# Kernel tuning notes

Hardware: AMD Instinct MI355X
Metric: run time of the kernel (lower is better)

## Reference

```python
import jax, jax.numpy as jnp
import numpy as np

B, L, D, H, DFF, C = 16, 1024, 256, 4, 2048, 3
NS, NC = 4, 4
DH = D // H


def _ln(x, g, b):
    m = x.mean(-1, keepdims=True)
    v = ((x - m) ** 2).mean(-1, keepdims=True)
    return (x - m) / jnp.sqrt(v + 1e-5) * g + b


def setup_inputs() -> dict:
    key = jax.random.key(0)
    ks = jax.random.split(key, 24)
    n = lambda k, s: jax.random.normal(k, s, jnp.float32) * 0.02
    return {
        'shape_idxs': jax.random.randint(ks[0], (B, L), 0, NS, jnp.int32),
        'color_idxs': jax.random.randint(ks[1], (B, L), 0, NC, jnp.int32),
        'shape_emb': n(ks[2], (NS, D)),
        'color_emb': n(ks[3], (NC, D)),
        'Wq': n(ks[4], (D, D)), 'bq': jnp.zeros((D,)),
        'Wk': n(ks[5], (D, D)), 'bk': jnp.zeros((D,)),
        'Wv': n(ks[6], (D, D)), 'bv': jnp.zeros((D,)),
        'Wo': n(ks[7], (D, D)), 'bo': jnp.zeros((D,)),
        'g1': jnp.ones((D,)), 'be1': jnp.zeros((D,)),
        'W1': n(ks[8], (D, DFF)), 'bf1': jnp.zeros((DFF,)),
        'W2': n(ks[9], (DFF, D)), 'bf2': jnp.zeros((D,)),
        'g2': jnp.ones((D,)), 'be2': jnp.zeros((D,)),
        'Wl': n(ks[10], (D, C)), 'bl': jnp.zeros((C,)),
        'Wp1': n(ks[11], (D, D)), 'bp1': jnp.zeros((D,)),
        'Wp2': n(ks[12], (D, 1)), 'bp2': jnp.zeros((1,)),
        'wc': n(ks[13], (1, 1)), 'bc': jnp.zeros((1,)),
    }


def reference(shape_idxs, color_idxs, shape_emb, color_emb, Wq, bq, Wk, bk, Wv, bv,
              Wo, bo, g1, be1, W1, bf1, W2, bf2, g2, be2, Wl, bl,
              Wp1, bp1, Wp2, bp2, wc, bc):
    # embed (dropout is identity in eval)
    x = shape_emb[shape_idxs] + color_emb[color_idxs]  # [B,L,D]
    # post-norm transformer encoder layer (PyTorch default)
    heads = lambda t: t.reshape(B, L, H, DH)
    q, k, v = heads(x @ Wq + bq), heads(x @ Wk + bk), heads(x @ Wv + bv)
    scores = jnp.einsum('blhd,bmhd->bhlm', q, k) / jnp.sqrt(jnp.float32(DH))
    attn = jax.nn.softmax(scores, axis=-1)
    ctx = jnp.einsum('bhlm,bmhd->blhd', attn, v).reshape(B, L, D)
    y = _ln(x + ctx @ Wo + bo, g1, be1)
    ff = jax.nn.relu(y @ W1 + bf1) @ W2 + bf2
    y = _ln(y + ff, g2, be2)  # trans_out [B,L,D]
    # latent logits / KL(prior || probs) with batchmean reduction
    logits = y @ Wl + bl
    logp = jax.nn.log_softmax(logits, axis=-1)
    prior = 1.0 / C
    kl_loss = jnp.sum(prior * (jnp.log(jnp.float32(prior)) - logp)) / B
    # data-dependent boundary segmentation (argmax of probs == argmax of logits)
    boundaries = (jnp.argmax(logits, axis=-1) == 0)
    boundaries = boundaries.at[:, 0].set(True)
    closed = boundaries & (jnp.arange(L) > 0)  # closure at l>0 ends segment at l
    seg_id = jnp.cumsum(closed.astype(jnp.int32), axis=1) - closed  # exclusive cumsum
    gid = (jnp.arange(B)[:, None] * L + seg_id).reshape(-1)  # global segment ids
    sums = jax.ops.segment_sum(y.reshape(B * L, D), gid, num_segments=B * L)
    counts = jax.ops.segment_sum(jnp.ones((B * L,), jnp.float32), gid, num_segments=B * L)
    means = sums / jnp.maximum(counts, 1.0)[:, None]  # per-segment mean [B*L,D]
    # predicate net + composition, mean over valid segments
    preds = jax.nn.sigmoid(jax.nn.relu(means @ Wp1 + bp1) @ Wp2 + bp2)  # [B*L,1]
    comp = (preds * wc[0, 0] + bc[0]).reshape(B, L)
    valid = (counts > 0).reshape(B, L).astype(jnp.float32)
    mean_comp = jnp.sum(comp * valid, axis=1) / jnp.sum(valid, axis=1)
    final_scores = jax.nn.sigmoid(mean_comp)
    return final_scores, kl_loss
```

## Files before the change

### kernel.cpp

```cpp
#include <hip/hip_runtime.h>


typedef unsigned short u16;
typedef u16    u16x4  __attribute__((ext_vector_type(4)));
typedef u16    u16x8  __attribute__((ext_vector_type(8)));
typedef __bf16 bf16x8 __attribute__((ext_vector_type(8)));
typedef float  f32x4  __attribute__((ext_vector_type(4)));

__device__ __forceinline__ float bf2f(u16 u) {
    union { unsigned int i; float f; } v; v.i = ((unsigned int)u) << 16; return v.f;
}
__device__ __forceinline__ u16 f2bf(float f) {
    union { float f; unsigned int i; } v; v.f = f;
    unsigned int r = (v.i + 0x7FFFu + ((v.i >> 16) & 1u)) >> 16;
    return (u16)r;
}
__device__ __forceinline__ u16 f2bf_fast(float f) {
    union { __bf16 h; u16 u; } v; v.h = (__bf16)f; return v.u;
}
__device__ __forceinline__ void gll16(const u16* g, u16* l) {
    __builtin_amdgcn_global_load_lds((__attribute__((address_space(1))) void*)(u16*)g,
                                     (__attribute__((address_space(3))) void*)l, 16, 0, 0);
}
__device__ __forceinline__ int get_mode(const int* __restrict__ detp) {
    int s = 0;
#pragma unroll 8
    for (int i = 0; i < 64; ++i) s += detp[i];
    return s > 16;
}

__global__ __launch_bounds__(256) void k_detect(const u16* __restrict__ w1raw,
                                                int* __restrict__ detp) {
    int i = blockIdx.x * 256 + threadIdx.x;
    int bad = 0;
    for (int k = i; k < 65536; k += 64 * 256) {
        unsigned v = w1raw[k] & 0x7FFFu;
        if (v >= 0x7F80u) bad++;
    }
    for (int off = 32; off >= 1; off >>= 1) bad += __shfl_xor(bad, off);
    __shared__ int bs[4];
    if ((threadIdx.x & 63) == 0) bs[threadIdx.x >> 6] = bad;
    __syncthreads();
    if (threadIdx.x == 0) detp[blockIdx.x] = bs[0] + bs[1] + bs[2] + bs[3];
}
__global__ void k_sentinel_f32(float* __restrict__ out, int code) {
    int t = threadIdx.x;
    if (t < 17) out[t] = (float)code;
}

struct PrepTab {
    const void* src[7];
    u16*        dst[7];
    int         K[7], N[7];
    float       scale[7];
    int         tstart[8];
    const void* isrc[17];
    unsigned    idstoff[17];
    int         in[17];
    float       iscale[17];
    u16*        ing;
};
__global__ __launch_bounds__(256) void k_prep(PrepTab tt, const int* __restrict__ detp) {
    int m = get_mode(detp);
    int bx = blockIdx.x;
    if (bx >= tt.tstart[7]) {
        int t = bx - tt.tstart[7];
        int n = tt.in[t];
        float sc = tt.iscale[t];
        u16* dst = tt.ing + tt.idstoff[t];
        for (int i = threadIdx.x; i < n; i += 256) {
            float v = m ? ((const float*)tt.isrc[t])[i] : bf2f(((const u16*)tt.isrc[t])[i]);
            dst[i] = f2bf(v * sc);
        }
        return;
    }
    __shared__ u16 tile[32][33];
    int wgt = 0;
#pragma unroll
    for (int i = 1; i < 7; ++i) if (bx >= tt.tstart[i]) wgt = i;
    int local = bx - tt.tstart[wgt];
    int K = tt.K[wgt], N = tt.N[wgt];
    float sc = tt.scale[wgt];
    int ntx = N >> 5;
    int txt = local % ntx, tyt = local / ntx;
    const void* W = tt.src[wgt];
    u16* Wt = tt.dst[wgt];
    int tx = threadIdx.x & 31, ty = threadIdx.x >> 5;
    int n = txt * 32 + tx;
    for (int i = ty; i < 32; i += 8) {
        size_t idx = (size_t)(tyt * 32 + i) * N + n;
        float v = m ? ((const float*)W)[idx] : bf2f(((const u16*)W)[idx]);
        tile[i][tx] = f2bf(v * sc);
    }
    __syncthreads();
    int k2 = tyt * 32 + tx;
    for (int i = ty; i < 32; i += 8) {
        int n2 = txt * 32 + i;
        Wt[(size_t)n2 * K + k2] = tile[tx][i];
    }
}

__global__ __launch_bounds__(256) void k_embed(const int* __restrict__ si,
                                               const int* __restrict__ ci,
                                               const void* __restrict__ se,
                                               const void* __restrict__ ce,
                                               u16* __restrict__ X,
                                               const int* __restrict__ detp) {
    int m = get_mode(detp);
    int t = blockIdx.x * 256 + threadIdx.x;
    int row = t >> 5, seg = (t & 31) * 8;
    int s = si[row], c = ci[row];
    u16x8 o;
    if (m) {
        const float* sp = (const float*)se + s * 256 + seg;
        const float* cp = (const float*)ce + c * 256 + seg;
#pragma unroll
        for (int e = 0; e < 8; ++e) o[e] = f2bf(sp[e] + cp[e]);
    } else {
        u16x8 a = *(const u16x8*)((const u16*)se + s * 256 + seg);
        u16x8 b = *(const u16x8*)((const u16*)ce + c * 256 + seg);
#pragma unroll
        for (int e = 0; e < 8; ++e) o[e] = f2bf(bf2f(a[e]) + bf2f(b[e]));
    }
    *(u16x8*)&X[(size_t)row * 256 + seg] = o;
}

__global__ __launch_bounds__(256) void k_gemm_bt(const u16* __restrict__ A,
                                                 const u16* __restrict__ Bt,
                                                 const u16* __restrict__ bias,
                                                 u16* __restrict__ C,
                                                 int N, int K, int relu, int gx) {
    __shared__ u16 As[128][32];
    __shared__ u16 Bs[128][32];
    const int tid = threadIdx.x;
    const int xcd = blockIdx.x & 7, j = blockIdx.x >> 3;
    const int m0 = (xcd * 16 + j / gx) * 128, n0 = (j % gx) * 128;
    const int lane = tid & 63, wid = tid >> 6;
    const int wm = (wid & 1) * 64, wn = (wid >> 1) * 64;
    const int m16 = lane & 15, quad = lane >> 4;
    f32x4 acc[4][4] = {};
    const int arow = tid >> 2;
    const int ac8  = (tid & 3) * 8;
    const u16* Ap0 = A  + (size_t)(m0 + arow) * K + ac8;
    const u16* Ap1 = A  + (size_t)(m0 + 64 + arow) * K + ac8;
    const u16* Bp0 = Bt + (size_t)(n0 + arow) * K + ac8;
    const u16* Bp1 = Bt + (size_t)(n0 + 64 + arow) * K + ac8;
    u16* lA0 = &As[arow][ac8];
    u16* lA1 = &As[64 + arow][ac8];
    u16* lB0 = &Bs[arow][ac8];
    u16* lB1 = &Bs[64 + arow][ac8];

    for (int k0 = 0; k0 < K; k0 += 32) {
        __syncthreads();
        gll16(Ap0 + k0, lA0);
        gll16(Ap1 + k0, lA1);
        gll16(Bp0 + k0, lB0);
        gll16(Bp1 + k0, lB1);
        __syncthreads();
        bf16x8 af[4], bfv[4];
#pragma unroll
        for (int i = 0; i < 4; ++i)
            af[i] = *(const bf16x8*)&As[wm + i * 16 + m16][quad * 8];
#pragma unroll
        for (int j2 = 0; j2 < 4; ++j2)
            bfv[j2] = *(const bf16x8*)&Bs[wn + j2 * 16 + m16][quad * 8];
#pragma unroll
        for (int i = 0; i < 4; ++i)
#pragma unroll
            for (int j2 = 0; j2 < 4; ++j2)
                acc[i][j2] = __builtin_amdgcn_mfma_f32_16x16x32_bf16(
                    af[i], bfv[j2], acc[i][j2], 0, 0, 0);
    }

#pragma unroll
    for (int i = 0; i < 4; ++i) {
        int row = m0 + wm + i * 16 + quad * 4;
#pragma unroll
        for (int j2 = 0; j2 < 4; ++j2) {
            int col = n0 + wn + j2 * 16 + m16;
            float bv = bf2f(bias[col]);
#pragma unroll
            for (int r = 0; r < 4; ++r) {
                float v = acc[i][j2][r] + bv;
                if (relu) v = fmaxf(v, 0.f);
                C[(size_t)(row + r) * N + col] = f2bf_fast(v);
            }
        }
    }
}

__global__ __launch_bounds__(256) void k_gemm64(const u16* __restrict__ A,
                                                const u16* __restrict__ Bt,
                                                const u16* __restrict__ bias,
                                                u16* __restrict__ C,
                                                int N, int K, int relu,
                                                int gx, int mtpx,
                                                u16* __restrict__ vt) {
    __shared__ u16 As0[64][32], As1[64][32];
    __shared__ u16 Bs0[128][32], Bs1[128][32];
    const int tid = threadIdx.x;
    const int xcd = blockIdx.x & 7, j = blockIdx.x >> 3;
    const int m0 = (xcd * mtpx + j / gx) * 64, n0 = (j % gx) * 128;
    const int vmode = (vt != nullptr) && (n0 >= 512);
    const int lane = tid & 63, wid = tid >> 6;
    const int wm = (wid & 1) * 32, wn = (wid >> 1) * 64;
    const int m16 = lane & 15, quad = lane >> 4;
    f32x4 acc[2][4] = {};
    const int arow = tid >> 2;
    const int ac8  = (tid & 3) * 8;
    const u16* Ap  = A  + (size_t)(m0 + arow) * K + ac8;
    const u16* Bp0 = Bt + (size_t)(n0 + arow) * K + ac8;
    const u16* Bp1 = Bt + (size_t)(n0 + 64 + arow) * K + ac8;
    u16* lA0  = &As0[arow][ac8];
    u16* lA1  = &As1[arow][ac8];
    u16* lB00 = &Bs0[arow][ac8];
    u16* lB01 = &Bs0[64 + arow][ac8];
    u16* lB10 = &Bs1[arow][ac8];
    u16* lB11 = &Bs1[64 + arow][ac8];

    for (int k0 = 0; k0 < K; k0 += 64) {
        __syncthreads();
        gll16(Ap + k0,        lA0);
        gll16(Ap + k0 + 32,   lA1);
        gll16(Bp0 + k0,       lB00);
        gll16(Bp0 + k0 + 32,  lB10);
        gll16(Bp1 + k0,       lB01);
        gll16(Bp1 + k0 + 32,  lB11);
        __syncthreads();
#pragma unroll
        for (int ks = 0; ks < 2; ++ks) {
            bf16x8 af[2], bfv[4];
#pragma unroll
            for (int i = 0; i < 2; ++i)
                af[i] = ks == 0 ? *(const bf16x8*)&As0[wm + i * 16 + m16][quad * 8]
                                : *(const bf16x8*)&As1[wm + i * 16 + m16][quad * 8];
#pragma unroll
            for (int j2 = 0; j2 < 4; ++j2)
                bfv[j2] = ks == 0 ? *(const bf16x8*)&Bs0[wn + j2 * 16 + m16][quad * 8]
                                  : *(const bf16x8*)&Bs1[wn + j2 * 16 + m16][quad * 8];
#pragma unroll
            for (int i = 0; i < 2; ++i)
#pragma unroll
                for (int j2 = 0; j2 < 4; ++j2)
                    acc[i][j2] = __builtin_amdgcn_mfma_f32_16x16x32_bf16(
                        af[i], bfv[j2], acc[i][j2], 0, 0, 0);
        }
    }

#pragma unroll
    for (int i = 0; i < 2; ++i) {
        int row = m0 + wm + i * 16 + quad * 4;
#pragma unroll
        for (int j2 = 0; j2 < 4; ++j2) {
            int col = n0 + wn + j2 * 16 + m16;
            float bv = bf2f(bias[col]);
            if (vmode) {
                int ch = col - 512;
                u16x4 o;
#pragma unroll
                for (int r = 0; r < 4; ++r) o[r] = f2bf_fast(acc[i][j2][r] + bv);
                size_t vb = ((size_t)((row >> 10) * 4 + (ch >> 6)) * 64 + (ch & 63)) * 1024
                          + (row & 1023);
                *(u16x4*)&vt[vb] = o;
            } else {
#pragma unroll
                for (int r = 0; r < 4; ++r) {
                    float v = acc[i][j2][r] + bv;
                    if (relu) v = fmaxf(v, 0.f);
                    C[(size_t)(row + r) * N + col] = f2bf_fast(v);
                }
            }
        }
    }
}

__global__ __launch_bounds__(256) void k_gemm64n(const u16* __restrict__ A,
                                                 const u16* __restrict__ Bt,
                                                 const u16* __restrict__ bias,
                                                 u16* __restrict__ C,
                                                 int N, int K, int relu,
                                                 int gnx, int mtpx,
                                                 const float* __restrict__ gate) {
    __shared__ u16 As0[64][32], As1[64][32];
    __shared__ u16 Bs0[64][32], Bs1[64][32];
    const int tid = threadIdx.x;
    const int xcd = blockIdx.x & 7, j = blockIdx.x >> 3;
    const int m0 = (xcd * mtpx + j / gnx) * 64, n0 = (j % gnx) * 64;
    if (gate && gate[m0] == 0.f) return;
    const int lane = tid & 63, w = tid >> 6;
    const int m16 = lane & 15, quad = lane >> 4;
    f32x4 acc[4] = {};
    const int arow = tid >> 2;
    const int ac8  = (tid & 3) * 8;
    const u16* Ap = A  + (size_t)(m0 + arow) * K + ac8;
    const u16* Bp = Bt + (size_t)(n0 + arow) * K + ac8;
    u16* lA0 = &As0[arow][ac8];
    u16* lA1 = &As1[arow][ac8];
    u16* lB0 = &Bs0[arow][ac8];
    u16* lB1 = &Bs1[arow][ac8];

    for (int k0 = 0; k0 < K; k0 += 64) {
        __syncthreads();
        gll16(Ap + k0,       lA0);
        gll16(Ap + k0 + 32,  lA1);
        gll16(Bp + k0,       lB0);
        gll16(Bp + k0 + 32,  lB1);
        __syncthreads();
#pragma unroll
        for (int ks = 0; ks < 2; ++ks) {
            bf16x8 af = ks == 0 ? *(const bf16x8*)&As0[w * 16 + m16][quad * 8]
                                : *(const bf16x8*)&As1[w * 16 + m16][quad * 8];
#pragma unroll
            for (int nt = 0; nt < 4; ++nt) {
                bf16x8 bfv = ks == 0 ? *(const bf16x8*)&Bs0[nt * 16 + m16][quad * 8]
                                     : *(const bf16x8*)&Bs1[nt * 16 + m16][quad * 8];
                acc[nt] = __builtin_amdgcn_mfma_f32_16x16x32_bf16(af, bfv, acc[nt], 0, 0, 0);
            }
        }
    }

#pragma unroll
    for (int nt = 0; nt < 4; ++nt) {
        int col = n0 + nt * 16 + m16;
        float bv = bf2f(bias[col]);
        int row = m0 + w * 16 + quad * 4;
#pragma unroll
        for (int r = 0; r < 4; ++r) {
            float v = acc[nt][r] + bv;
            if (relu) v = fmaxf(v, 0.f);
            C[(size_t)(row + r) * N + col] = f2bf_fast(v);
        }
    }
}

__global__ __launch_bounds__(256) void k_attn_mfma(const u16* __restrict__ QKV,
                                                   const u16* __restrict__ VT,
                                                   u16* __restrict__ CTX) {
    __shared__ u16 Ks[64][72];
    __shared__ u16 Vts[64][72];
    __shared__ u16 Ps[4][16][72];
    const int tid = threadIdx.x, lane = tid & 63, w = tid >> 6;
    const int quad = lane >> 4, c = lane & 15;
    const int blk = blockIdx.x;
    const int xcd = blk & 7, local = blk >> 3;
    const int bh = xcd * 8 + (local >> 4);
    const int qt = local & 15;
    const int b = bh >> 2, h = bh & 3;
    const int qrow0 = b * 1024 + qt * 64;

    const u16* qptr = QKV + (size_t)(qrow0 + w * 16 + c) * 768 + h * 64;
    bf16x8 aq0 = *(const bf16x8*)(qptr + quad * 8);
    bf16x8 aq1 = *(const bf16x8*)(qptr + 32 + quad * 8);

    bf16x8 ones;
    {
        union { u16 u; __bf16 h; } v; v.u = 0x3F80;
#pragma unroll
        for (int e = 0; e < 8; ++e) ones[e] = v.h;
    }

    f32x4 acc_o[4] = {};
    f32x4 acc_l = {};

    const u16* kbase  = QKV + (size_t)(b * 1024) * 768 + 256 + h * 64;
    const u16* vtbase = VT + (size_t)(bh * 64) * 1024;
    const int skk = tid >> 3, sc8 = (tid & 7) * 8;

    for (int t = 0; t < 16; ++t) {
        __syncthreads();
#pragma unroll
        for (int it = 0; it < 2; ++it) {
            int rr = skk + 32 * it;
            *(u16x8*)&Ks[rr][sc8]  = *(const u16x8*)(kbase + (size_t)(t * 64 + rr) * 768 + sc8);
            *(u16x8*)&Vts[rr][sc8] = *(const u16x8*)(vtbase + (size_t)rr * 1024 + t * 64 + sc8);
        }
        __syncthreads();

        f32x4 s[4];
#pragma unroll
        for (int nt = 0; nt < 4; ++nt) {
            f32x4 z = {};
            bf16x8 bk0 = *(const bf16x8*)&Ks[nt * 16 + c][quad * 8];
            bf16x8 bk1 = *(const bf16x8*)&Ks[nt * 16 + c][32 + quad * 8];
            z = __builtin_amdgcn_mfma_f32_16x16x32_bf16(aq0, bk0, z, 0, 0, 0);
            s[nt] = __builtin_amdgcn_mfma_f32_16x16x32_bf16(aq1, bk1, z, 0, 0, 0);
        }

#pragma unroll
        for (int nt = 0; nt < 4; ++nt)
#pragma unroll
            for (int r = 0; r < 4; ++r)
                Ps[w][quad * 4 + r][nt * 16 + c] = f2bf_fast(exp2f(fminf(s[nt][r], 80.f)));

#pragma unroll
        for (int ks = 0; ks < 2; ++ks) {
            bf16x8 ap = *(const bf16x8*)&Ps[w][c][ks * 32 + quad * 8];
            acc_l = __builtin_amdgcn_mfma_f32_16x16x32_bf16(ap, ones, acc_l, 0, 0, 0);
#pragma unroll
            for (int nt = 0; nt < 4; ++nt) {
                bf16x8 bv = *(const bf16x8*)&Vts[nt * 16 + c][ks * 32 + quad * 8];
                acc_o[nt] = __builtin_amdgcn_mfma_f32_16x16x32_bf16(ap, bv, acc_o[nt], 0, 0, 0);
            }
        }
    }

#pragma unroll
    for (int nt = 0; nt < 4; ++nt) {
        int col = h * 64 + nt * 16 + c;
#pragma unroll
        for (int r = 0; r < 4; ++r) {
            int row = qrow0 + w * 16 + quad * 4 + r;
            CTX[(size_t)row * 256 + col] = f2bf_fast(acc_o[nt][r] / acc_l[r]);
        }
    }
}

__global__ __launch_bounds__(256) void k_ln(const u16* __restrict__ A,
                                            const u16* __restrict__ R,
                                            const u16* __restrict__ g,
                                            const u16* __restrict__ be,
                                            u16* __restrict__ out) {
    int w = threadIdx.x >> 6, lane = threadIdx.x & 63;
    int row = blockIdx.x * 4 + w;
    size_t base = (size_t)row * 256 + lane * 4;
    u16x4 a4 = *(const u16x4*)&A[base];
    u16x4 r4 = *(const u16x4*)&R[base];
    float v[4];
    float s = 0.f, sq = 0.f;
#pragma unroll
    for (int j = 0; j < 4; ++j) {
        v[j] = bf2f(a4[j]) + bf2f(r4[j]);
        s += v[j]; sq += v[j] * v[j];
    }
    for (int off = 32; off >= 1; off >>= 1) { s += __shfl_xor(s, off); sq += __shfl_xor(sq, off); }
    float mean = s * (1.f / 256.f);
    float var  = sq * (1.f / 256.f) - mean * mean;
    float rs   = rsqrtf(var + 1e-5f);
    u16x4 o;
#pragma unroll
    for (int j = 0; j < 4; ++j) {
        int d = lane * 4 + j;
        o[j] = f2bf((v[j] - mean) * rs * bf2f(g[d]) + bf2f(be[d]));
    }
    *(u16x4*)&out[base] = o;
}

__global__ __launch_bounds__(256) void k_logits(const u16* __restrict__ FFO,
                                                const u16* __restrict__ Y1,
                                                const u16* __restrict__ g2,
                                                const u16* __restrict__ be2,
                                                const u16* __restrict__ Wl,
                                                const u16* __restrict__ bl,
                                                u16* __restrict__ Y2,
                                                float* __restrict__ klpart,
                                                int* __restrict__ flags) {
    const int tid = threadIdx.x, lane = tid & 63, w = tid >> 6;
    float wv[4][3], gv[4], bev[4];
#pragma unroll
    for (int j = 0; j < 4; ++j) {
        int d = lane * 4 + j;
        gv[j]  = bf2f(g2[d]);
        bev[j] = bf2f(be2[d]);
#pragma unroll
        for (int c = 0; c < 3; ++c) wv[j][c] = bf2f(Wl[d * 3 + c]);
    }
    const float b0 = bf2f(bl[0]), b1 = bf2f(bl[1]), b2 = bf2f(bl[2]);
    float klsum = 0.f;
    const int row0 = blockIdx.x * 16 + w * 4;
    for (int i = 0; i < 4; ++i) {
        int row = row0 + i;
        size_t base = (size_t)row * 256 + lane * 4;
        u16x4 f4 = *(const u16x4*)&FFO[base];
        u16x4 y4 = *(const u16x4*)&Y1[base];
        float v[4];
        float s = 0.f, sq = 0.f;
#pragma unroll
        for (int j = 0; j < 4; ++j) {
            v[j] = bf2f(f4[j]) + bf2f(y4[j]);
            s += v[j]; sq += v[j] * v[j];
        }
        for (int off = 32; off >= 1; off >>= 1) { s += __shfl_xor(s, off); sq += __shfl_xor(sq, off); }
        float mean = s * (1.f / 256.f);
        float var  = sq * (1.f / 256.f) - mean * mean;
        float rs   = rsqrtf(var + 1e-5f);
        u16x4 o;
        float a0 = 0.f, a1 = 0.f, a2 = 0.f;
#pragma unroll
        for (int j = 0; j < 4; ++j) {
            float yn = (v[j] - mean) * rs * gv[j] + bev[j];
            o[j] = f2bf(yn);
            float y = bf2f(o[j]);
            a0 += y * wv[j][0]; a1 += y * wv[j][1]; a2 += y * wv[j][2];
        }
        *(u16x4*)&Y2[base] = o;
        for (int off = 32; off >= 1; off >>= 1) {
            a0 += __shfl_xor(a0, off); a1 += __shfl_xor(a1, off); a2 += __shfl_xor(a2, off);
        }
        if (lane == 0) {
            float l0 = a0 + b0, l1 = a1 + b1, l2 = a2 + b2;
            float mx = fmaxf(l0, fmaxf(l1, l2));
            float lse = mx + __logf(__expf(l0 - mx) + __expf(l1 - mx) + __expf(l2 - mx));
            klsum += lse - (l0 + l1 + l2) * (1.f / 3.f) - 1.0986122886681098f;
            int am = 0; float bv = l0;
            if (l1 > bv) { bv = l1; am = 1; }
            if (l2 > bv) { am = 2; }
            int l = row & 1023;
            flags[row] = (am == 0 && l != 0) ? 1 : 0;
        }
    }
    __shared__ float kls[4];
    if (lane == 0) kls[w] = klsum;
    __syncthreads();
    if (tid == 0) klpart[blockIdx.x] = kls[0] + kls[1] + kls[2] + kls[3];
}

__global__ void k_scan(const int* __restrict__ flags, int* __restrict__ seg) {
    __shared__ int wsum[16];
    int b = blockIdx.x, t = threadIdx.x;
    int lane = t & 63, w = t >> 6;
    int f = flags[b * 1024 + t];
    int x = f;
#pragma unroll
    for (int off = 1; off < 64; off <<= 1) {
        int v = __shfl_up(x, off);
        if (lane >= off) x += v;
    }
    if (lane == 63) wsum[w] = x;
    __syncthreads();
    if (w == 0) {
        int s = (lane < 16) ? wsum[lane] : 0;
#pragma unroll
        for (int off = 1; off < 16; off <<= 1) {
            int v = __shfl_up(s, off);
            if (lane >= off) s += v;
        }
        if (lane < 16) wsum[lane] = s;
    }
    __syncthreads();
    int prefix = (w > 0) ? wsum[w - 1] : 0;
    seg[b * 1024 + t] = prefix + x - f;
}

__global__ __launch_bounds__(64) void k_segmean(const u16* __restrict__ Y,
                                                const int* __restrict__ seg,
                                                u16* __restrict__ means,
                                                float* __restrict__ cnt) {
    int g = blockIdx.x, lane = threadIdx.x;
    int b = g >> 10, s = g & 1023;
    const int* sb = seg + b * 1024;
    int target = s + (lane & 1);
    int lo = 0, hi = 1024;
    while (lo < hi) {
        int mid = (lo + hi) >> 1;
        if (sb[mid] < target) lo = mid + 1; else hi = mid;
    }
    int start = __shfl(lo, 0);
    int end   = __shfl(lo, 1);
    int n = end - start;
    if (lane == 0) cnt[g] = (float)n;
    if (n <= 0) return;
    f32x4 acc = {};
    for (int row = start; row < end; ++row) {
        u16x4 y4 = *(const u16x4*)&Y[(size_t)(b * 1024 + row) * 256 + lane * 4];
        acc[0] += bf2f(y4[0]); acc[1] += bf2f(y4[1]);
        acc[2] += bf2f(y4[2]); acc[3] += bf2f(y4[3]);
    }
    float inv = 1.f / (float)n;
    u16x4 o;
#pragma unroll
    for (int j = 0; j < 4; ++j) o[j] = f2bf(acc[j] * inv);
    *(u16x4*)&means[(size_t)g * 256 + lane * 4] = o;
}

__global__ __launch_bounds__(256) void k_preds(const u16* __restrict__ T,
                                               const u16* __restrict__ Wp2,
                                               const u16* __restrict__ bp2,
                                               const u16* __restrict__ wc,
                                               const u16* __restrict__ bc,
                                               const float* __restrict__ cnt,
                                               float* __restrict__ predp) {
    const int tid = threadIdx.x, lane = tid & 63, w = tid >> 6;
    float lwp[4];
#pragma unroll
    for (int j = 0; j < 4; ++j) lwp[j] = bf2f(Wp2[lane * 4 + j]);
    const float fb = bf2f(bp2[0]), fw = bf2f(wc[0]), fc = bf2f(bc[0]);
    float csum = 0.f, vsum = 0.f;
    const int g0 = blockIdx.x * 16 + w * 4;
    if (cnt[g0] != 0.f) {
        for (int i = 0; i < 4; ++i) {
            int g = g0 + i;
            u16x4 t4 = *(const u16x4*)&T[(size_t)g * 256 + lane * 4];
            float a = 0.f;
#pragma unroll
            for (int j = 0; j < 4; ++j) a += bf2f(t4[j]) * lwp[j];
            for (int off = 32; off >= 1; off >>= 1) a += __shfl_xor(a, off);
            if (lane == 0 && cnt[g] > 0.f) {
                float pred = 1.f / (1.f + __expf(-(a + fb)));
                csum += pred * fw + fc;
                vsum += 1.f;
            }
        }
    }
    __shared__ float cs[4], vs[4];
    if (lane == 0) { cs[w] = csum; vs[w] = vsum; }
    __syncthreads();
    if (tid == 0) {
        predp[2 * blockIdx.x]     = cs[0] + cs[1] + cs[2] + cs[3];
        predp[2 * blockIdx.x + 1] = vs[0] + vs[1] + vs[2] + vs[3];
    }
}

__global__ void k_final(const float* __restrict__ predp, const float* __restrict__ klp,
                        const int* __restrict__ detp, void* __restrict__ outv) {
    int t = threadIdx.x;
    float k = 0.f;
    for (int i = t; i < 1024; i += 64) k += klp[i];
    for (int off = 32; off >= 1; off >>= 1) k += __shfl_xor(k, off);
    float ktot = __shfl(k, 0);
    int batch = t >> 2, ch = t & 3;
    float c = 0.f, v = 0.f;
    for (int i = 0; i < 16; ++i) {
        int blk = batch * 64 + ch * 16 + i;
        c += predp[2 * blk];
        v += predp[2 * blk + 1];
    }
    c += __shfl_xor(c, 1); c += __shfl_xor(c, 2);
    v += __shfl_xor(v, 1); v += __shfl_xor(v, 2);
    int mode = get_mode(detp);
    if ((t & 3) == 0) {
        float d = v, nm = c;
        if (!(d > 0.f)) d = 1.f;
        if (isnan(nm) || isinf(nm)) nm = 0.f;
        float val = 1.f / (1.f + __expf(-nm / d));
        if (mode) ((float*)outv)[batch] = val;
        else      ((u16*)outv)[batch]   = f2bf(val);
    }
    if (t == 1) {
        float val = ktot * (1.f / 16.f);
        if (isnan(val) || isinf(val)) val = 0.f;
        if (mode) ((float*)outv)[16] = val;
        else      ((u16*)outv)[16]   = f2bf(val);
    }
}

extern "C" void kernel_launch(void* const* d_in, const int* in_sizes, int n_in,
                              void* d_out, int out_size, void* d_ws, size_t ws_size,
                              hipStream_t stream) {
    const int* shape_idxs = (const int*)d_in[0];
    const int* color_idxs = (const int*)d_in[1];
    char* ws = (char*)d_ws;
    const size_t MB = 1024 * 1024;

    if (ws_size < 90 * MB) {
        int wsMB = (int)(ws_size >> 20); if (wsMB > 250) wsMB = 250;
        k_sentinel_f32<<<1, 32, 0, stream>>>((float*)d_out, 200 + wsMB);
        return;
    }

    u16*   X     = (u16*)(ws);
    u16*   QKVb  = (u16*)(ws + 8 * MB);
    u16*   VT    = (u16*)(ws + 32 * MB);
    u16*   CTX   = (u16*)(ws + 40 * MB);
    u16*   CTXP  = (u16*)(ws + 48 * MB);
    u16*   Y1    = (u16*)(ws + 64 * MB);
    u16*   Hb    = (u16*)(ws);
    u16*   FFO   = (u16*)(ws + 72 * MB);
    u16*   Y2    = (u16*)(ws);
    u16*   MEANS = (u16*)(ws + 24 * MB);
    u16*   TB    = (u16*)(ws + 32 * MB);
    int*   FLAGS = (int*)(ws + 80 * MB);
    int*   SEG   = (int*)(ws + 80 * MB + 65536);
    float* CNT   = (float*)(ws + 80 * MB + 131072);
    float* KLP   = (float*)(ws + 80 * MB + 262144);
    float* PREDP = (float*)(ws + 80 * MB + 327680);
    u16*   W3T   = (u16*)(ws + 81 * MB);
    u16*   WoT   = (u16*)(ws + 81 * MB + 786432);
    u16*   Wp1T  = (u16*)(ws + 81 * MB + 917504);
    u16*   W1T   = (u16*)(ws + 82 * MB);
    u16*   W2T   = (u16*)(ws + 83 * MB);
    int*   DETP  = (int*)(ws + 84 * MB);
    u16*   ING   = (u16*)(ws + 85 * MB);

    const float QSCALE = 0.125f * 1.44269504f;

    PrepTab tt;
    const void* tsrc[7] = {d_in[4], d_in[6], d_in[8], d_in[10], d_in[22], d_in[14], d_in[16]};
    u16* tdst[7] = {W3T, W3T + 256 * 256, W3T + 512 * 256, WoT, Wp1T, W1T, W2T};
    int tK[7] = {256, 256, 256, 256, 256, 256, 2048};
    int tN[7] = {256, 256, 256, 256, 256, 2048, 256};
    int ts = 0;
    for (int i = 0; i < 7; ++i) {
        tt.src[i] = tsrc[i]; tt.dst[i] = tdst[i]; tt.K[i] = tK[i]; tt.N[i] = tN[i];
        tt.scale[i] = (i == 0) ? QSCALE : 1.0f;
        tt.tstart[i] = ts;
        ts += (tK[i] >> 5) * (tN[i] >> 5);
    }
    tt.tstart[7] = ts;

    static const int II[17]  = {5, 7, 9, 11, 12, 13, 15, 17, 18, 19, 20, 21, 23, 24, 25, 26, 27};
    static const int IN[17]  = {256, 256, 256, 256, 256, 256, 2048, 256, 256, 256, 768, 3, 256, 256, 1, 1, 1};
    unsigned off = 0;
    for (int i = 0; i < 17; ++i) {
        tt.isrc[i] = d_in[II[i]];
        tt.in[i] = IN[i];
        tt.iscale[i] = 1.0f;
        if (i == 0) { tt.idstoff[0] = off; off += 768; }
        else if (i == 1) tt.idstoff[1] = tt.idstoff[0] + 256;
        else if (i == 2) tt.idstoff[2] = tt.idstoff[0] + 512;
        else { tt.idstoff[i] = off; off += (unsigned)((IN[i] + 8) & ~7); }
    }
    tt.iscale[0] = QSCALE;
    tt.ing = ING;
    const u16* ib3  = ING + tt.idstoff[0];
    const u16* ibo  = ING + tt.idstoff[3];
    const u16* ig1  = ING + tt.idstoff[4];  const u16* ibe1 = ING + tt.idstoff[5];
    const u16* ibf1 = ING + tt.idstoff[6];  const u16* ibf2 = ING + tt.idstoff[7];
    const u16* ig2  = ING + tt.idstoff[8];  const u16* ibe2 = ING + tt.idstoff[9];
    const u16* iWl  = ING + tt.idstoff[10]; const u16* ibl  = ING + tt.idstoff[11];
    const u16* ibp1 = ING + tt.idstoff[12]; const u16* iWp2 = ING + tt.idstoff[13];
    const u16* ibp2 = ING + tt.idstoff[14]; const u16* iwc  = ING + tt.idstoff[15];
    const u16* ibc  = ING + tt.idstoff[16];

    k_detect<<<64, 256, 0, stream>>>((const u16*)d_in[14], DETP);
    k_prep<<<ts + 17, 256, 0, stream>>>(tt, DETP);
    k_embed<<<2048, 256, 0, stream>>>(shape_idxs, color_idxs, d_in[2], d_in[3], X, DETP);
    k_gemm64<<<1536, 256, 0, stream>>>(X, W3T, ib3, QKVb, 768, 256, 0, 6, 32, VT);
    k_attn_mfma<<<1024, 256, 0, stream>>>(QKVb, VT, CTX);
    k_gemm64n<<<1024, 256, 0, stream>>>(CTX, WoT, ibo, CTXP, 256, 256, 0, 4, 32, nullptr);
    k_ln<<<4096, 256, 0, stream>>>(CTXP, X, ig1, ibe1, Y1);
    k_gemm_bt<<<16 * 128, 256, 0, stream>>>(Y1, W1T, ibf1, Hb, 2048, 256, 1, 16);
    k_gemm64n<<<1024, 256, 0, stream>>>(Hb, W2T, ibf2, FFO, 256, 2048, 0, 4, 32, nullptr);
    k_logits<<<1024, 256, 0, stream>>>(FFO, Y1, ig2, ibe2, iWl, ibl, Y2, KLP, FLAGS);
    k_scan<<<16, 1024, 0, stream>>>(FLAGS, SEG);
    k_segmean<<<16384, 64, 0, stream>>>(Y2, SEG, MEANS, CNT);
    k_gemm64n<<<1024, 256, 0, stream>>>(MEANS, Wp1T, ibp1, TB, 256, 256, 1, 4, 32, CNT);
    k_preds<<<1024, 256, 0, stream>>>(TB, iWp2, ibp2, iwc, ibc, CNT, PREDP);
    k_final<<<1, 64, 0, stream>>>(PREDP, KLP, DETP, d_out);
}
```

Measured before the change: 301.3 us.

## Compute transposed scores in registers to skip LDS round-trip for P

Swaps the operands of the QK^T MFMA so each lane's S^T output directly forms the A-operand fragment for the PV MFMA. K rows are written to LDS with a row-permuting swizzle so that the output layout matches. This removes the Ps shared buffer and its write/read round-trip per tile, which saves LDS traffic and shared memory. The cost is a more intricate index mapping that must stay consistent with the MFMA layouts.

After: 301.1 us. About the same (-0.1%).

```diff
diff --git a/kernel.cpp b/kernel.cpp
--- a/kernel.cpp
+++ b/kernel.cpp
@@ -338,7 +338,6 @@
                                                    u16* __restrict__ CTX) {
     __shared__ u16 Ks[64][72];
     __shared__ u16 Vts[64][72];
-    __shared__ u16 Ps[4][16][72];
     const int tid = threadIdx.x, lane = tid & 63, w = tid >> 6;
     const int quad = lane >> 4, c = lane & 15;
     const int blk = blockIdx.x;
@@ -365,36 +364,40 @@
     const u16* kbase  = QKV + (size_t)(b * 1024) * 768 + 256 + h * 64;
     const u16* vtbase = VT + (size_t)(bh * 64) * 1024;
     const int skk = tid >> 3, sc8 = (tid & 7) * 8;
+    const int swk = (skk & ~12) | ((skk & 4) << 1) | ((skk & 8) >> 1);
+    const int sra = ((c & 8) << 1) | (c & 4) | (c & 3);
 
     for (int t = 0; t < 16; ++t) {
         __syncthreads();
 #pragma unroll
         for (int it = 0; it < 2; ++it) {
             int rr = skk + 32 * it;
-            *(u16x8*)&Ks[rr][sc8]  = *(const u16x8*)(kbase + (size_t)(t * 64 + rr) * 768 + sc8);
+            *(u16x8*)&Ks[swk + 32 * it][sc8] =
+                *(const u16x8*)(kbase + (size_t)(t * 64 + rr) * 768 + sc8);
             *(u16x8*)&Vts[rr][sc8] = *(const u16x8*)(vtbase + (size_t)rr * 1024 + t * 64 + sc8);
         }
         __syncthreads();
 
-        f32x4 s[4];
-#pragma unroll
-        for (int nt = 0; nt < 4; ++nt) {
-            f32x4 z = {};
-            bf16x8 bk0 = *(const bf16x8*)&Ks[nt * 16 + c][quad * 8];
-            bf16x8 bk1 = *(const bf16x8*)&Ks[nt * 16 + c][32 + quad * 8];
-            z = __builtin_amdgcn_mfma_f32_16x16x32_bf16(aq0, bk0, z, 0, 0, 0);
-            s[nt] = __builtin_amdgcn_mfma_f32_16x16x32_bf16(aq1, bk1, z, 0, 0, 0);
-        }
-
-#pragma unroll
-        for (int nt = 0; nt < 4; ++nt)
-#pragma unroll
-            for (int r = 0; r < 4; ++r)
-                Ps[w][quad * 4 + r][nt * 16 + c] = f2bf_fast(exp2f(fminf(s[nt][r], 80.f)));
-
 #pragma unroll
         for (int ks = 0; ks < 2; ++ks) {
-            bf16x8 ap = *(const bf16x8*)&Ps[w][c][ks * 32 + quad * 8];
+            const int ra = ks * 32 + sra;
+            bf16x8 ka0 = *(const bf16x8*)&Ks[ra][quad * 8];
+            bf16x8 ka1 = *(const bf16x8*)&Ks[ra][32 + quad * 8];
+            bf16x8 kb0 = *(const bf16x8*)&Ks[ra + 8][quad * 8];
+            bf16x8 kb1 = *(const bf16x8*)&Ks[ra + 8][32 + quad * 8];
+            f32x4 za = {}, zb = {};
+            za = __builtin_amdgcn_mfma_f32_16x16x32_bf16(ka0, aq0, za, 0, 0, 0);
+            za = __builtin_amdgcn_mfma_f32_16x16x32_bf16(ka1, aq1, za, 0, 0, 0);
+            zb = __builtin_amdgcn_mfma_f32_16x16x32_bf16(kb0, aq0, zb, 0, 0, 0);
+            zb = __builtin_amdgcn_mfma_f32_16x16x32_bf16(kb1, aq1, zb, 0, 0, 0);
+
+            bf16x8 ap;
+#pragma unroll
+            for (int r = 0; r < 4; ++r) {
+                ap[r]     = (__bf16)exp2f(fminf(za[r], 80.f));
+                ap[4 + r] = (__bf16)exp2f(fminf(zb[r], 80.f));
+            }
+
             acc_l = __builtin_amdgcn_mfma_f32_16x16x32_bf16(ap, ones, acc_l, 0, 0, 0);
 #pragma unroll
             for (int nt = 0; nt < 4; ++nt) {
```
